# Kernel optimization log

Measured on AMD Instinct MI355X. Metric: run time of the kernel, lower is better.

The kernel has to match this reference:

```python
import jax, jax.numpy as jnp
import numpy as np

L, B, DM, H, HID, NSPK, NB, NC, WIN = 128, 64, 1024, 256, 256, 2, 30, 6, 10
F = 2 * H            # biLSTM output feature dim
MEM = F + HID        # concat of node features and graph-conv output
R = 2 * NSPK * NSPK  # number of edge relations


def _build_edges():
    src_l, dst_l = [], []
    for j in range(L):
        for k in range(max(0, j - WIN), min(L, j + WIN + 1)):
            dst_l.append(j); src_l.append(k)
    dst = np.asarray(dst_l, np.int32); src = np.asarray(src_l, np.int32)
    offs = (np.arange(B, dtype=np.int32) * L)[:, None]
    edge_dst = (dst[None] + offs).reshape(-1)
    edge_src = (src[None] + offs).reshape(-1)
    mask = np.zeros((L, L), bool); mask[dst, src] = True
    return edge_src, edge_dst, mask


def setup_inputs():
    key = jax.random.key(0)
    ks = iter(jax.random.split(key, 32))
    rn = lambda *s: jax.random.normal(next(ks), s, jnp.float32) * 0.05
    edge_src, edge_dst, edge_mask = _build_edges()
    return {
        'U': jax.random.normal(next(ks), (L, B, DM), jnp.float32),
        'umask': jnp.ones((B, L), jnp.float32),
        'Wih0': rn(2, 4 * H, DM), 'Whh0': rn(2, 4 * H, H), 'b0': rn(2, 4 * H),
        'Wih1': rn(2, 4 * H, F), 'Whh1': rn(2, 4 * H, H), 'b1': rn(2, 4 * H),
        'W_scalar': rn(F, L),
        'basis': rn(NB, F, HID), 'comp': rn(R, NB),
        'W_root': rn(F, HID), 'b_rgcn': rn(HID),
        'gc_W1': rn(HID, HID), 'gc_W2': rn(HID, HID), 'gc_b': rn(HID),
        'Wm': rn(MEM, MEM), 'bm': rn(MEM),
        'Wl': rn(MEM, HID), 'bl': rn(HID),
        'Ws': rn(HID, NC), 'bs': rn(NC),
        'speakers': jax.random.randint(next(ks), (L, B), 0, NSPK, jnp.int32),
        'edge_src': jnp.asarray(edge_src), 'edge_dst': jnp.asarray(edge_dst),
        'edge_mask': jnp.asarray(edge_mask),
    }


def _lstm_dir(x, Wih, Whh, b, reverse):
    Bx, Hh = x.shape[1], Whh.shape[1]
    def step(carry, xt):
        h, c = carry
        g = xt @ Wih.T + h @ Whh.T + b          # PyTorch gate order i,f,g,o
        i, f, gg, o = jnp.split(g, 4, axis=-1)
        c = jax.nn.sigmoid(f) * c + jax.nn.sigmoid(i) * jnp.tanh(gg)
        h = jax.nn.sigmoid(o) * jnp.tanh(c)
        return (h, c), h
    init = (jnp.zeros((Bx, Hh), x.dtype), jnp.zeros((Bx, Hh), x.dtype))
    return jax.lax.scan(step, init, x, reverse=reverse)[1]


def _bilstm(x, Wih, Whh, b):
    return jnp.concatenate([_lstm_dir(x, Wih[0], Whh[0], b[0], False),
                            _lstm_dir(x, Wih[1], Whh[1], b[1], True)], -1)


def reference(U, umask, Wih0, Whh0, b0, Wih1, Whh1, b1, W_scalar, basis, comp,
              W_root, b_rgcn, gc_W1, gc_W2, gc_b, Wm, bm, Wl, bl, Ws, bs,
              speakers, edge_src, edge_dst, edge_mask):
    # --- 2-layer biLSTM encoder ---
    feats = _bilstm(_bilstm(U, Wih0, Whh0, b0), Wih1, Whh1, b1)   # (L,B,F)
    # --- MaskedEdgeAttention ('attn1'): edge weights ---
    scale = jnp.einsum('sbd,dm->sbm', feats, W_scalar)            # (L,B,L)
    alpha = jax.nn.softmax(scale, axis=0).transpose(1, 2, 0)      # (B,Lt,Ls)
    masked = alpha * jnp.where(edge_mask, 1.0, 1e-10)
    scores = masked / masked.sum(-1, keepdims=True) * edge_mask
    b_idx = edge_dst // L; i0 = edge_dst % L; i1 = edge_src % L
    edge_norm = scores[b_idx, i0, i1]                             # (E,)
    # --- edge types: speaker pair + temporal direction ---
    s_dst = speakers[i0, b_idx]; s_src = speakers[i1, b_idx]
    e_dir = jnp.where(i0 < i1, 0, 1)
    edge_type = s_dst * (2 * NSPK) + s_src * 2 + e_dir            # (E,) in [0,R)
    # --- node features, conversation-major ---
    x = feats.transpose(1, 0, 2).reshape(B * L, F)                # (N,F)
    N = B * L
    # --- RGCNConv with basis decomposition ---
    W_rel = jnp.einsum('rb,bfo->rfo', comp, basis)                # (R,F,HID)
    x_rel = jnp.einsum('nf,rfo->nro', x, W_rel)                   # (N,R,HID)
    msg = x_rel[edge_src, edge_type] * edge_norm[:, None]
    h = jax.ops.segment_sum(msg, edge_dst, num_segments=N) + x @ W_root + b_rgcn
    # --- GraphConv ---
    agg = jax.ops.segment_sum(h[edge_src], edge_dst, num_segments=N)
    h2 = h @ gc_W1 + gc_b + agg @ gc_W2                           # (N,HID)
    em = jnp.concatenate([x, h2], -1)                             # (N,MEM)
    em = em.reshape(B, L, MEM).transpose(1, 0, 2)                 # (L,B,MEM)
    # --- MatchingAttention ('general2') at every timestep, vectorized ---
    um = umask.T                                                  # (L,B)
    x_tr = em @ Wm + bm                                           # (L,B,MEM)
    logits = jnp.einsum('tbm,sbm->tbs', x_tr, em * um[:, :, None]) * umask[None]
    a = jax.nn.softmax(jnp.tanh(logits), axis=2) * umask[None]
    a = a / a.sum(2, keepdims=True)
    att = jnp.einsum('tbs,sbm->tbm', a, em)
    hidden = jax.nn.relu(att @ Wl + bl)                           # dropout = eval identity
    logp = jax.nn.log_softmax(hidden @ Ws + bs, axis=2)           # (L,B,NC)
    return logp.transpose(1, 0, 2).reshape(B * L, NC)
```

## Files before the change

kernel.cpp:

```cpp
#include <hip/hip_runtime.h>
#include <cstdint>


typedef __attribute__((ext_vector_type(8))) short bf16x8;
typedef __attribute__((ext_vector_type(4))) float f32x4;

__device__ __forceinline__ void gload_lds16(const void* g, void* l) {
  __builtin_amdgcn_global_load_lds(
      (const __attribute__((address_space(1))) void*)g,
      (__attribute__((address_space(3))) void*)l, 16, 0, 0);
}

template<bool HASBIAS, bool ACCUM, bool RELU, bool OUTBF>
__global__ __launch_bounds__(256) void gemm_bf16_nt(
    const ushort* __restrict__ A, const ushort* __restrict__ Bt,
    const float* __restrict__ bias, void* __restrict__ Cv,
    int M, int N, int K, long lda, long ldc,
    long sA, long sB, long sC, long sBias)
{
  const int bz = blockIdx.z;
  A += (long)bz * sA;
  Bt += (long)bz * sB;
  if (HASBIAS) bias += (long)bz * sBias;
  float*  Cf = OUTBF ? nullptr : ((float*)Cv + (long)bz * sC);
  ushort* Cb = OUTBF ? ((ushort*)Cv + (long)bz * sC) : nullptr;

  const int bn = blockIdx.x * 128, bm = blockIdx.y * 128;

  __shared__ ushort As[128][32];
  __shared__ ushort Bs[128][32];

  const int tid = threadIdx.x;
  const int wave = tid >> 6, lane = tid & 63;
  const int wm = (wave >> 1) * 64, wn = (wave & 1) * 64;
  const int fr = lane & 15;
  const int fk = (lane >> 4) * 8;

  f32x4 acc[4][4];
#pragma unroll
  for (int i = 0; i < 4; ++i)
#pragma unroll
    for (int j = 0; j < 4; ++j) acc[i][j] = (f32x4){0.f, 0.f, 0.f, 0.f};

  const int f0 = wave * 2 * 64 + lane;
  const int f1 = f0 + 64;
  const int r0 = f0 >> 2, c0 = (f0 & 3) * 8;
  const int r1 = f1 >> 2, c1 = (f1 & 3) * 8;
  ushort* As0 = (ushort*)As + wave * 2 * 512;
  ushort* As1 = As0 + 512;
  ushort* Bs0 = (ushort*)Bs + wave * 2 * 512;
  ushort* Bs1 = Bs0 + 512;

  for (int k0 = 0; k0 < K; k0 += 32) {
    gload_lds16(A + (long)(bm + r0) * lda + k0 + c0, As0);
    gload_lds16(A + (long)(bm + r1) * lda + k0 + c1, As1);
    gload_lds16(Bt + (long)(bn + r0) * K + k0 + c0, Bs0);
    gload_lds16(Bt + (long)(bn + r1) * K + k0 + c1, Bs1);
    __syncthreads();

    bf16x8 af[4], bfr[4];
#pragma unroll
    for (int f = 0; f < 4; ++f) {
      af[f]  = *(const bf16x8*)&As[wm + f * 16 + fr][fk];
      bfr[f] = *(const bf16x8*)&Bs[wn + f * 16 + fr][fk];
    }
#pragma unroll
    for (int mf = 0; mf < 4; ++mf)
#pragma unroll
      for (int nf = 0; nf < 4; ++nf)
        acc[mf][nf] = __builtin_amdgcn_mfma_f32_16x16x32_bf16(
            af[mf], bfr[nf], acc[mf][nf], 0, 0, 0);
    __syncthreads();
  }

  float bv[4];
#pragma unroll
  for (int nf = 0; nf < 4; ++nf)
    bv[nf] = HASBIAS ? bias[bn + wn + nf * 16 + fr] : 0.f;

  const int crow0 = (lane >> 4) * 4;
#pragma unroll
  for (int mf = 0; mf < 4; ++mf)
#pragma unroll
    for (int r = 0; r < 4; ++r) {
      const long roff = (long)(bm + wm + mf * 16 + crow0 + r) * ldc + bn + wn;
#pragma unroll
      for (int nf = 0; nf < 4; ++nf) {
        float v = acc[mf][nf][r] + bv[nf];
        if (OUTBF) {
          unsigned u = __float_as_uint(v);
          u += 0x7fffu + ((u >> 16) & 1u);
          Cb[roff + nf * 16 + fr] = (ushort)(u >> 16);
        } else {
          if (ACCUM) v += Cf[roff + nf * 16 + fr];
          if (RELU) v = fmaxf(v, 0.f);
          Cf[roff + nf * 16 + fr] = v;
        }
      }
    }
}

__device__ __forceinline__ unsigned short f2bf(float f) {
  unsigned u = __float_as_uint(f);
  u += 0x7fffu + ((u >> 16) & 1u);
  return (unsigned short)(u >> 16);
}
__device__ __forceinline__ float bf2f(ushort v) {
  return __uint_as_float(((unsigned)v) << 16);
}
__device__ __forceinline__ float fast_sig(float x) {
  return __builtin_amdgcn_rcpf(1.f + __expf(-x));
}
__device__ __forceinline__ float fast_tanh(float x) {
  return 2.f * fast_sig(2.f * x) - 1.f;
}

__device__ __forceinline__ int sdot4_(uint a, uint b, int c) {
#if __has_builtin(__builtin_amdgcn_sdot4)
  return __builtin_amdgcn_sdot4((int)a, (int)b, c, false);
#else
  int r = c;
  r += ((int)(a << 24) >> 24) * ((int)(b << 24) >> 24);
  r += ((int)(a << 16) >> 24) * ((int)(b << 16) >> 24);
  r += ((int)(a << 8)  >> 24) * ((int)(b << 8)  >> 24);
  r += ((int)a >> 24)         * ((int)b >> 24);
  return r;
#endif
}

__global__ __launch_bounds__(256) void cvt_all_k(
    const float* __restrict__ U, ushort* __restrict__ ubf,
    const float* __restrict__ W0, ushort* __restrict__ w0,
    const float* __restrict__ W1, ushort* __restrict__ w1,
    const float* __restrict__ b_rgcn, float* __restrict__ biasSW)
{
  const int bid = blockIdx.x;
  if (bid >= 11264) {
    const int idx = (bid - 11264) * 256 + threadIdx.x;
    if (idx < 384) biasSW[idx] = (idx < 128) ? 0.f : b_rgcn[idx - 128];
    return;
  }
  const float* src; ushort* dst; long base;
  if (bid < 8192)       { src = U;  dst = ubf; base = (long)bid * 1024; }
  else if (bid < 10240) { src = W0; dst = w0;  base = (long)(bid - 8192) * 1024; }
  else                  { src = W1; dst = w1;  base = (long)(bid - 10240) * 1024; }
  const long i = base + threadIdx.x * 4;
  float4 v = *(const float4*)(src + i);
  ushort4 o;
  o.x = f2bf(v.x); o.y = f2bf(v.y); o.z = f2bf(v.z); o.w = f2bf(v.w);
  *(ushort4*)(dst + i) = o;
}

__global__ __launch_bounds__(256) void tp_all_k(
    const float* __restrict__ s0, ushort* __restrict__ d0,
    const float* __restrict__ s1, const float* __restrict__ s2,
    ushort* __restrict__ d12,
    const float* __restrict__ s3, ushort* __restrict__ d3,
    const float* __restrict__ s4, ushort* __restrict__ d4,
    const float* __restrict__ s5, ushort* __restrict__ d5)
{
  __shared__ float tile[32][33];
  const int bid = blockIdx.x;
  const float* src; ushort* dst; int C, gx, local, dstStride, dstOff;
  if (bid < 128)       { src = s0; dst = d0;  C = 256; gx = 8;  local = bid;        dstStride = 512; dstOff = 0; }
  else if (bid < 192)  { src = s1; dst = d12; C = 256; gx = 8;  local = bid - 128;  dstStride = 512; dstOff = 0; }
  else if (bid < 256)  { src = s2; dst = d12; C = 256; gx = 8;  local = bid - 192;  dstStride = 512; dstOff = 256; }
  else if (bid < 832)  { src = s3; dst = d3;  C = 768; gx = 24; local = bid - 256;  dstStride = 768; dstOff = 0; }
  else if (bid < 1024) { src = s4; dst = d4;  C = 256; gx = 8;  local = bid - 832;  dstStride = 768; dstOff = 0; }
  else                 { src = s5; dst = d5;  C = 128; gx = 4;  local = bid - 1024; dstStride = 512; dstOff = 0; }
  const int c0 = (local % gx) * 32, r0 = (local / gx) * 32;
  const int tx = threadIdx.x & 31, ty = threadIdx.x >> 5;
#pragma unroll
  for (int j = 0; j < 4; ++j)
    tile[ty + j * 8][tx] = src[(long)(r0 + ty + j * 8) * C + c0 + tx];
  __syncthreads();
#pragma unroll
  for (int j = 0; j < 4; ++j)
    dst[(long)(c0 + ty + j * 8) * dstStride + dstOff + r0 + tx] = f2bf(tile[tx][ty + j * 8]);
}

__global__ __launch_bounds__(256) void pack_whh_all_k(
    const float* __restrict__ Whh0, const float* __restrict__ Whh1,
    uint* __restrict__ Wq, float* __restrict__ fscale)
{
  const int wid = (blockIdx.x * 256 + threadIdx.x) >> 6;
  const int lane = threadIdx.x & 63;
  const int l = wid >> 11;
  const int wid2 = wid & 2047;
  const int d = wid2 >> 10, gi = wid2 & 1023;
  const float* Whh = l ? Whh1 : Whh0;
  const float* row = Whh + ((long)d * 1024 + gi) * 256 + lane * 4;
  float v0 = row[0], v1 = row[1], v2 = row[2], v3 = row[3];
  float am = fmaxf(fmaxf(fabsf(v0), fabsf(v1)), fmaxf(fabsf(v2), fabsf(v3)));
#pragma unroll
  for (int off = 32; off > 0; off >>= 1) am = fmaxf(am, __shfl_xor(am, off, 64));
  am = fmaxf(am, 1e-12f);
  const float inv = 127.f / am;
  int q0 = __float2int_rn(v0 * inv), q1 = __float2int_rn(v1 * inv);
  int q2 = __float2int_rn(v2 * inv), q3 = __float2int_rn(v3 * inv);
  uint w = (uint)(q0 & 255) | ((uint)(q1 & 255) << 8) |
           ((uint)(q2 & 255) << 16) | ((uint)(q3 & 255) << 24);
  Wq[(long)l * 131072 + ((long)d * 64 + lane) * 1024 + gi] = w;
  if (lane == 0) fscale[l * 2048 + d * 1024 + gi] = am / 127.f;
}

__global__ __launch_bounds__(1024) void lstm4_k(
    const ushort* __restrict__ Xg,
    const uint* __restrict__ Wq,
    const float* __restrict__ fscale,
    ushort* __restrict__ out,
    int bmajor, long ldo)
{
  const int bx = blockIdx.x;
  const int d = bx >> 6, b = bx & 63;
  const int tid = threadIdx.x;

  __shared__ uint hq[2][64];
  __shared__ float preactF[1024];

  uint w[64];
  const uint* wrow = Wq + (long)d * 65536 + tid;
#pragma unroll
  for (int k4 = 0; k4 < 64; ++k4) w[k4] = wrow[k4 * 1024];

  if (tid < 128) ((uint*)hq)[tid] = 0u;

  const float fsc = fscale[d * 1024 + tid] * (1.0f / 127.0f);
  const ushort* Xd = Xg + (long)d * 8192 * 1024;

  float c = 0.f;
  float x0 = 0.f, x1 = 0.f, x2 = 0.f, x3 = 0.f;
  if (tid < 256) {
    const ushort* xr = Xd + ((long)((d ? 127 : 0) * 64 + b)) * 1024;
    x0 = bf2f(xr[tid]); x1 = bf2f(xr[tid + 256]);
    x2 = bf2f(xr[tid + 512]); x3 = bf2f(xr[tid + 768]);
  }
  __syncthreads();

  int cur = 0;
  for (int step = 0; step < 128; ++step) {
    const int t = d ? 127 - step : step;

    float n0 = 0.f, n1 = 0.f, n2 = 0.f, n3 = 0.f;
    if (tid < 256 && step + 1 < 128) {
      const ushort* xr = Xd + ((long)((d ? 126 - step : step + 1) * 64 + b)) * 1024;
      n0 = bf2f(xr[tid]); n1 = bf2f(xr[tid + 256]);
      n2 = bf2f(xr[tid + 512]); n3 = bf2f(xr[tid + 768]);
    }

    int acc = 0;
    const uint4* hrow = (const uint4*)hq[cur];
#pragma unroll
    for (int k16 = 0; k16 < 16; ++k16) {
      uint4 h4 = hrow[k16];
      acc = sdot4_(w[k16 * 4 + 0], h4.x, acc);
      acc = sdot4_(w[k16 * 4 + 1], h4.y, acc);
      acc = sdot4_(w[k16 * 4 + 2], h4.z, acc);
      acc = sdot4_(w[k16 * 4 + 3], h4.w, acc);
    }
    preactF[tid] = (float)acc * fsc;
    __syncthreads();

    if (tid < 256) {
      float p0 = x0 + preactF[tid];
      float p1 = x1 + preactF[tid + 256];
      float p2 = x2 + preactF[tid + 512];
      float p3 = x3 + preactF[tid + 768];
      const float ig = fast_sig(p0), fg = fast_sig(p1);
      const float gg = fast_tanh(p2), og = fast_sig(p3);
      c = fg * c + ig * gg;
      const float h = og * fast_tanh(c);
      const long row = bmajor ? ((long)b * 128 + t) : ((long)t * 64 + b);
      out[row * ldo + (d << 8) + tid] = f2bf(h);
      ((char*)hq[cur ^ 1])[tid] = (char)__float2int_rn(h * 127.f);
      x0 = n0; x1 = n1; x2 = n2; x3 = n3;
    }
    __syncthreads();
    cur ^= 1;
  }
}

__global__ __launch_bounds__(256) void wrel_k(const float* __restrict__ basis,
                                              const float* __restrict__ comp,
                                              ushort* __restrict__ wrel2t) {
  const int f = blockIdx.x;
  const int o = threadIdx.x;
  __shared__ float cs[240];
  if (o < 240) cs[o] = comp[o];
  __syncthreads();
  float acc[8];
#pragma unroll
  for (int r = 0; r < 8; ++r) acc[r] = 0.f;
  for (int bb = 0; bb < 30; ++bb) {
    const float v = basis[((long)bb * 512 + f) * 256 + o];
#pragma unroll
    for (int r = 0; r < 8; ++r) acc[r] = fmaf(cs[r * 30 + bb], v, acc[r]);
  }
#pragma unroll
  for (int r = 0; r < 8; ++r)
    wrel2t[((long)(r * 256 + o)) * 512 + f] = f2bf(acc[r]);
}

__global__ __launch_bounds__(256) void rgcn_fused_k(
    const float* __restrict__ scaleM, const ushort* __restrict__ xrel,
    const int* __restrict__ spk, ushort* __restrict__ hagg)
{
  const int n = blockIdx.x;
  const int b = n >> 7, t = n & 127;
  const int o = threadIdx.x;
  const int lo = max(t - 10, 0), hi = min(t + 10, 127);
  const int cnt = hi - lo + 1;

  __shared__ float sc[128], red[128];
  __shared__ int spks[21];
  __shared__ int spkt_s;

  if (o < 128) {
    const float v = scaleM[((long)(b * 128 + o)) * 384 + t];
    sc[o] = v; red[o] = v;
  }
  if (o == 0) spkt_s = spk[t * 64 + b];
  if (o >= 128 && o - 128 < cnt) spks[o - 128] = spk[(lo + o - 128) * 64 + b];
  __syncthreads();
  for (int off = 64; off > 0; off >>= 1) {
    if (o < off) red[o] = fmaxf(red[o], red[o + off]);
    __syncthreads();
  }
  const float m = red[0];
  __syncthreads();
  if (o < 128) {
    const float e = expf(sc[o] - m);
    sc[o] = e;
    const int dd = o - t;
    const bool inwin = (dd <= 10) && (dd >= -10);
    red[o] = e * (inwin ? 1.0f : 1e-10f);
  }
  __syncthreads();
  for (int off = 64; off > 0; off >>= 1) {
    if (o < off) red[o] += red[o + off];
    __syncthreads();
  }
  const float inv_msum = 1.0f / red[0];
  __syncthreads();

  const int spkt = spkt_s;
  float acc = scaleM[(long)n * 384 + 128 + o];
  for (int q = 0; q < cnt; ++q) {
    const int s = lo + q;
    const float wv = sc[s] * inv_msum;
    const int et = spkt * 4 + spks[q] * 2 + ((t < s) ? 0 : 1);
    acc = fmaf(bf2f(xrel[(((long)(b * 128 + s)) * 8 + et) * 256 + o]), wv, acc);
  }
  hagg[(long)n * 512 + o] = f2bf(acc);
}

__global__ __launch_bounds__(256) void agg_k(ushort* __restrict__ hagg) {
  const int n = blockIdx.x;
  const int b = n >> 7, t = n & 127;
  const int o = threadIdx.x;
  const int lo = max(t - 10, 0), hi = min(t + 10, 127);
  float acc = 0.f;
  for (int s = lo; s <= hi; ++s) acc += bf2f(hagg[((long)(b * 128 + s)) * 512 + o]);
  hagg[(long)n * 512 + 256 + o] = f2bf(acc);
}

__global__ __launch_bounds__(256) void emt_k(const ushort* __restrict__ src,
                                             ushort* __restrict__ dst) {
  __shared__ ushort tile[32][33];
  const int c0 = blockIdx.x * 32;
  const int r0 = blockIdx.y * 32;
  const int b = blockIdx.z;
  const ushort* s = src + (long)b * 98304;
  ushort* d = dst + (long)b * 98304;
  const int tx = threadIdx.x & 31, ty = threadIdx.x >> 5;
#pragma unroll
  for (int j = 0; j < 4; ++j)
    tile[ty + j * 8][tx] = s[(long)(r0 + ty + j * 8) * 768 + c0 + tx];
  __syncthreads();
#pragma unroll
  for (int j = 0; j < 4; ++j)
    d[(long)(c0 + ty + j * 8) * 128 + r0 + tx] = tile[tx][ty + j * 8];
}

__global__ __launch_bounds__(128) void match_softmax_k(const float* __restrict__ logits,
                                                       const float* __restrict__ umask,
                                                       ushort* __restrict__ abf) {
  const int bx = blockIdx.x;
  const int b = bx >> 7;
  const int s = threadIdx.x;
  __shared__ float red[128];
  const float* row = logits + (long)bx * 128;
  const float um = umask[b * 128 + s];
  const float v = tanhf(row[s] * um * um);
  red[s] = v; __syncthreads();
  for (int off = 64; off > 0; off >>= 1) { if (s < off) red[s] = fmaxf(red[s], red[s + off]); __syncthreads(); }
  const float m = red[0]; __syncthreads();
  const float e = expf(v - m);
  red[s] = e; __syncthreads();
  for (int off = 64; off > 0; off >>= 1) { if (s < off) red[s] += red[s + off]; __syncthreads(); }
  const float es = red[0]; __syncthreads();
  const float p = (e / es) * um;
  red[s] = p; __syncthreads();
  for (int off = 64; off > 0; off >>= 1) { if (s < off) red[s] += red[s + off]; __syncthreads(); }
  const float ps = red[0];
  abf[(long)bx * 128 + s] = f2bf(p / ps);
}

__global__ __launch_bounds__(256) void final_k(const float* __restrict__ hidden,
                                               const float* __restrict__ Ws,
                                               const float* __restrict__ bs,
                                               float* __restrict__ out) {
  __shared__ float wsl[256 * 6];
  const int tid = threadIdx.x;
#pragma unroll
  for (int j = 0; j < 6; ++j) wsl[tid * 6 + j] = Ws[tid * 6 + j];
  __syncthreads();
  const int wave = tid >> 6, lane = tid & 63;
  const int n = blockIdx.x * 4 + wave;
  const float4 hv = *(const float4*)&hidden[(long)n * 256 + lane * 4];
  const float hvv[4] = {hv.x, hv.y, hv.z, hv.w};
  float a[6];
#pragma unroll
  for (int c = 0; c < 6; ++c) a[c] = 0.f;
#pragma unroll
  for (int j = 0; j < 4; ++j)
#pragma unroll
    for (int c = 0; c < 6; ++c)
      a[c] = fmaf(hvv[j], wsl[(lane * 4 + j) * 6 + c], a[c]);
#pragma unroll
  for (int off = 32; off > 0; off >>= 1)
#pragma unroll
    for (int c = 0; c < 6; ++c)
      a[c] += __shfl_xor(a[c], off, 64);
  if (lane == 0) {
    float v[6], m = -1e30f;
#pragma unroll
    for (int c = 0; c < 6; ++c) { v[c] = a[c] + bs[c]; m = fmaxf(m, v[c]); }
    float sum = 0.f;
#pragma unroll
    for (int c = 0; c < 6; ++c) sum += expf(v[c] - m);
    const float lse = m + logf(sum);
#pragma unroll
    for (int c = 0; c < 6; ++c) out[(long)n * 6 + c] = v[c] - lse;
  }
}

extern "C" void kernel_launch(void* const* d_in, const int* in_sizes, int n_in,
                              void* d_out, int out_size, void* d_ws, size_t ws_size,
                              hipStream_t stream) {
  const float* U        = (const float*)d_in[0];
  const float* umask    = (const float*)d_in[1];
  const float* Wih0     = (const float*)d_in[2];
  const float* Whh0     = (const float*)d_in[3];
  const float* b0       = (const float*)d_in[4];
  const float* Wih1     = (const float*)d_in[5];
  const float* Whh1     = (const float*)d_in[6];
  const float* b1       = (const float*)d_in[7];
  const float* W_scalar = (const float*)d_in[8];
  const float* basis    = (const float*)d_in[9];
  const float* comp     = (const float*)d_in[10];
  const float* W_root   = (const float*)d_in[11];
  const float* b_rgcn   = (const float*)d_in[12];
  const float* gc_W1    = (const float*)d_in[13];
  const float* gc_W2    = (const float*)d_in[14];
  const float* gc_b     = (const float*)d_in[15];
  const float* Wm       = (const float*)d_in[16];
  const float* bm       = (const float*)d_in[17];
  const float* Wl       = (const float*)d_in[18];
  const float* bl       = (const float*)d_in[19];
  const float* Wsw      = (const float*)d_in[20];
  const float* bsw      = (const float*)d_in[21];
  const int*   speakers = (const int*)d_in[22];

  float* ws = (float*)d_ws;
  float* gates   = ws + 0L;
  float* feats   = ws + 16777216L;
  float* xbuf    = ws + 20971520L;
  float* feats0  = ws + 25165824L;
  float* scaleb  = ws + 29360128L;
  float* scoresb = ws + 30408704L;
  float* wrelr   = ws + 31457280L;
  uint*  wq      = (uint*)(ws + 34603008L);
  float* fsc     = ws + 34865152L;
  float* wTr     = ws + 34869248L;
  float* biasSW  = ws + 35426304L;

  ushort* ubf    = (ushort*)xbuf;
  ushort* wih0bf = (ushort*)feats;
  ushort* wih1bf = (ushort*)(feats + 1048576L);
  ushort* f0bf   = (ushort*)feats0;
  ushort* xemb   = (ushort*)feats0;
  ushort* wrel2t = (ushort*)wrelr;
  ushort* wswr   = (ushort*)wTr;
  ushort* gcW12t = wswr + 196608L;
  ushort* Wmt    = gcW12t + 131072L;
  ushort* Wlt    = Wmt + 589824L;

  ushort* gatesbf = (ushort*)gates;
  float*  scaleM  = gates + 8388608L;
  ushort* hagg    = (ushort*)xbuf;
  ushort* emT     = (ushort*)xbuf;
  ushort* xrelbf  = (ushort*)gates;
  ushort* xtrbf   = (ushort*)gates;
  ushort* abf     = (ushort*)scoresb;
  ushort* attbf   = (ushort*)feats;

  float*  logitsb = scaleb;
  float*  hiddenb = scaleb;

  pack_whh_all_k<<<1024, 256, 0, stream>>>(Whh0, Whh1, wq, fsc);
  cvt_all_k<<<11266, 256, 0, stream>>>(U, ubf, Wih0, wih0bf, Wih1, wih1bf,
                                       b_rgcn, biasSW);
  tp_all_k<<<1088, 256, 0, stream>>>(W_root, wswr + 65536L, gc_W1, gc_W2, gcW12t,
                                     Wm, Wmt, Wl, Wlt, W_scalar, wswr);
  wrel_k<<<512, 256, 0, stream>>>(basis, comp, wrel2t);

  gemm_bf16_nt<true, false, false, true><<<dim3(8, 64, 2), 256, 0, stream>>>(
      ubf, wih0bf, b0, gatesbf, 8192, 1024, 1024, 1024L, 1024L,
      0L, 1048576L, 8388608L, 1024L);
  lstm4_k<<<128, 1024, 0, stream>>>(gatesbf, wq, fsc, f0bf, 0, 512L);

  gemm_bf16_nt<true, false, false, true><<<dim3(8, 64, 2), 256, 0, stream>>>(
      f0bf, wih1bf, b1, gatesbf, 8192, 1024, 512, 512L, 1024L,
      0L, 524288L, 8388608L, 1024L);
  lstm4_k<<<128, 1024, 0, stream>>>(gatesbf, wq + 131072, fsc + 2048, xemb, 1, 768L);

  gemm_bf16_nt<true, false, false, false><<<dim3(3, 64, 1), 256, 0, stream>>>(
      xemb, wswr, biasSW, scaleM, 8192, 384, 512, 768L, 384L, 0L, 0L, 0L, 0L);
  gemm_bf16_nt<false, false, false, true><<<dim3(16, 64, 1), 256, 0, stream>>>(
      xemb, wrel2t, nullptr, xrelbf, 8192, 2048, 512, 768L, 2048L, 0L, 0L, 0L, 0L);
  rgcn_fused_k<<<8192, 256, 0, stream>>>(scaleM, xrelbf, speakers, hagg);

  agg_k<<<8192, 256, 0, stream>>>(hagg);
  gemm_bf16_nt<true, false, false, true><<<dim3(2, 64, 1), 256, 0, stream>>>(
      hagg, gcW12t, gc_b, xemb + 512, 8192, 256, 512, 512L, 768L, 0L, 0L, 0L, 0L);

  gemm_bf16_nt<true, false, false, true><<<dim3(6, 64, 1), 256, 0, stream>>>(
      xemb, Wmt, bm, xtrbf, 8192, 768, 768, 768L, 768L, 0L, 0L, 0L, 0L);
  emt_k<<<dim3(24, 4, 64), 256, 0, stream>>>(xemb, emT);
  gemm_bf16_nt<false, false, false, false><<<dim3(1, 1, 64), 256, 0, stream>>>(
      xtrbf, xemb, nullptr, logitsb, 128, 128, 768, 768L, 128L,
      98304L, 98304L, 16384L, 0L);
  match_softmax_k<<<8192, 128, 0, stream>>>(logitsb, umask, abf);
  gemm_bf16_nt<false, false, false, true><<<dim3(6, 1, 64), 256, 0, stream>>>(
      abf, emT, nullptr, attbf, 128, 768, 128, 128L, 768L,
      16384L, 98304L, 98304L, 0L);

  gemm_bf16_nt<true, false, true, false><<<dim3(2, 64, 1), 256, 0, stream>>>(
      attbf, Wlt, bl, hiddenb, 8192, 256, 768, 768L, 256L, 0L, 0L, 0L, 0L);
  final_k<<<2048, 256, 0, stream>>>(hiddenb, Wsw, bsw, (float*)d_out);
}
```

Baseline: 584.1 us.

## Fuse matching attention into one per-batch kernel and merge prep kernels

Replaces the logits GEMM, the row softmax kernel and the attention GEMM with one kernel per batch element. Each block computes the logits with MFMA, keeps them in shared memory, applies the masked softmax there, and multiplies by emT without sending logits or weights through global memory. The four weight-preparation kernels are also merged into two launches to cut launch overhead. The fused attention runs only 64 blocks with large LDS use, so it may under-use the GPU compared with the separate kernels.

```diff
diff --git a/kernel.cpp b/kernel.cpp
--- a/kernel.cpp
+++ b/kernel.cpp
@@ -128,30 +128,58 @@
 #endif
 }
 
-__global__ __launch_bounds__(256) void cvt_all_k(
+__global__ __launch_bounds__(256) void prep1_k(
+    const float* __restrict__ Whh0, const float* __restrict__ Whh1,
+    uint* __restrict__ Wq, float* __restrict__ fscale,
+    const float* __restrict__ basis, const float* __restrict__ comp,
+    ushort* __restrict__ wrel2t)
+{
+  __shared__ float cs[240];
+  const int bid = blockIdx.x;
+  if (bid < 1024) {
+    const int wid = (bid * 256 + threadIdx.x) >> 6;
+    const int lane = threadIdx.x & 63;
+    const int l = wid >> 11;
+    const int wid2 = wid & 2047;
+    const int d = wid2 >> 10, gi = wid2 & 1023;
+    const float* Whh = l ? Whh1 : Whh0;
+    const float* row = Whh + ((long)d * 1024 + gi) * 256 + lane * 4;
+    float v0 = row[0], v1 = row[1], v2 = row[2], v3 = row[3];
+    float am = fmaxf(fmaxf(fabsf(v0), fabsf(v1)), fmaxf(fabsf(v2), fabsf(v3)));
+#pragma unroll
+    for (int off = 32; off > 0; off >>= 1) am = fmaxf(am, __shfl_xor(am, off, 64));
+    am = fmaxf(am, 1e-12f);
+    const float inv = 127.f / am;
+    int q0 = __float2int_rn(v0 * inv), q1 = __float2int_rn(v1 * inv);
+    int q2 = __float2int_rn(v2 * inv), q3 = __float2int_rn(v3 * inv);
+    uint w = (uint)(q0 & 255) | ((uint)(q1 & 255) << 8) |
+             ((uint)(q2 & 255) << 16) | ((uint)(q3 & 255) << 24);
+    Wq[(long)l * 131072 + ((long)d * 64 + lane) * 1024 + gi] = w;
+    if (lane == 0) fscale[l * 2048 + d * 1024 + gi] = am / 127.f;
+    return;
+  }
+  const int f = bid - 1024;
+  const int o = threadIdx.x;
+  if (o < 240) cs[o] = comp[o];
+  __syncthreads();
+  float acc[8];
+#pragma unroll
+  for (int r = 0; r < 8; ++r) acc[r] = 0.f;
+  for (int bb = 0; bb < 30; ++bb) {
+    const float v = basis[((long)bb * 512 + f) * 256 + o];
+#pragma unroll
+    for (int r = 0; r < 8; ++r) acc[r] = fmaf(cs[r * 30 + bb], v, acc[r]);
+  }
+#pragma unroll
+  for (int r = 0; r < 8; ++r)
+    wrel2t[((long)(r * 256 + o)) * 512 + f] = f2bf(acc[r]);
+}
+
+__global__ __launch_bounds__(256) void prep2_k(
     const float* __restrict__ U, ushort* __restrict__ ubf,
     const float* __restrict__ W0, ushort* __restrict__ w0,
     const float* __restrict__ W1, ushort* __restrict__ w1,
-    const float* __restrict__ b_rgcn, float* __restrict__ biasSW)
-{
-  const int bid = blockIdx.x;
-  if (bid >= 11264) {
-    const int idx = (bid - 11264) * 256 + threadIdx.x;
-    if (idx < 384) biasSW[idx] = (idx < 128) ? 0.f : b_rgcn[idx - 128];
-    return;
-  }
-  const float* src; ushort* dst; long base;
-  if (bid < 8192)       { src = U;  dst = ubf; base = (long)bid * 1024; }
-  else if (bid < 10240) { src = W0; dst = w0;  base = (long)(bid - 8192) * 1024; }
-  else                  { src = W1; dst = w1;  base = (long)(bid - 10240) * 1024; }
-  const long i = base + threadIdx.x * 4;
-  float4 v = *(const float4*)(src + i);
-  ushort4 o;
-  o.x = f2bf(v.x); o.y = f2bf(v.y); o.z = f2bf(v.z); o.w = f2bf(v.w);
-  *(ushort4*)(dst + i) = o;
-}
-
-__global__ __launch_bounds__(256) void tp_all_k(
+    const float* __restrict__ b_rgcn, float* __restrict__ biasSW,
     const float* __restrict__ s0, ushort* __restrict__ d0,
     const float* __restrict__ s1, const float* __restrict__ s2,
     ushort* __restrict__ d12,
@@ -160,7 +188,25 @@
     const float* __restrict__ s5, ushort* __restrict__ d5)
 {
   __shared__ float tile[32][33];
-  const int bid = blockIdx.x;
+  const int bid0 = blockIdx.x;
+  if (bid0 < 11264) {
+    const float* src; ushort* dst; long base;
+    if (bid0 < 8192)       { src = U;  dst = ubf; base = (long)bid0 * 1024; }
+    else if (bid0 < 10240) { src = W0; dst = w0;  base = (long)(bid0 - 8192) * 1024; }
+    else                   { src = W1; dst = w1;  base = (long)(bid0 - 10240) * 1024; }
+    const long i = base + threadIdx.x * 4;
+    float4 v = *(const float4*)(src + i);
+    ushort4 o;
+    o.x = f2bf(v.x); o.y = f2bf(v.y); o.z = f2bf(v.z); o.w = f2bf(v.w);
+    *(ushort4*)(dst + i) = o;
+    return;
+  }
+  if (bid0 < 11266) {
+    const int idx = (bid0 - 11264) * 256 + threadIdx.x;
+    if (idx < 384) biasSW[idx] = (idx < 128) ? 0.f : b_rgcn[idx - 128];
+    return;
+  }
+  const int bid = bid0 - 11266;
   const float* src; ushort* dst; int C, gx, local, dstStride, dstOff;
   if (bid < 128)       { src = s0; dst = d0;  C = 256; gx = 8;  local = bid;        dstStride = 512; dstOff = 0; }
   else if (bid < 192)  { src = s1; dst = d12; C = 256; gx = 8;  local = bid - 128;  dstStride = 512; dstOff = 0; }
@@ -177,31 +223,6 @@
 #pragma unroll
   for (int j = 0; j < 4; ++j)
     dst[(long)(c0 + ty + j * 8) * dstStride + dstOff + r0 + tx] = f2bf(tile[tx][ty + j * 8]);
-}
-
-__global__ __launch_bounds__(256) void pack_whh_all_k(
-    const float* __restrict__ Whh0, const float* __restrict__ Whh1,
-    uint* __restrict__ Wq, float* __restrict__ fscale)
-{
-  const int wid = (blockIdx.x * 256 + threadIdx.x) >> 6;
-  const int lane = threadIdx.x & 63;
-  const int l = wid >> 11;
-  const int wid2 = wid & 2047;
-  const int d = wid2 >> 10, gi = wid2 & 1023;
-  const float* Whh = l ? Whh1 : Whh0;
-  const float* row = Whh + ((long)d * 1024 + gi) * 256 + lane * 4;
-  float v0 = row[0], v1 = row[1], v2 = row[2], v3 = row[3];
-  float am = fmaxf(fmaxf(fabsf(v0), fabsf(v1)), fmaxf(fabsf(v2), fabsf(v3)));
-#pragma unroll
-  for (int off = 32; off > 0; off >>= 1) am = fmaxf(am, __shfl_xor(am, off, 64));
-  am = fmaxf(am, 1e-12f);
-  const float inv = 127.f / am;
-  int q0 = __float2int_rn(v0 * inv), q1 = __float2int_rn(v1 * inv);
-  int q2 = __float2int_rn(v2 * inv), q3 = __float2int_rn(v3 * inv);
-  uint w = (uint)(q0 & 255) | ((uint)(q1 & 255) << 8) |
-           ((uint)(q2 & 255) << 16) | ((uint)(q3 & 255) << 24);
-  Wq[(long)l * 131072 + ((long)d * 64 + lane) * 1024 + gi] = w;
-  if (lane == 0) fscale[l * 2048 + d * 1024 + gi] = am / 127.f;
 }
 
 __global__ __launch_bounds__(1024) void lstm4_k(
@@ -280,27 +301,6 @@
   }
 }
 
-__global__ __launch_bounds__(256) void wrel_k(const float* __restrict__ basis,
-                                              const float* __restrict__ comp,
-                                              ushort* __restrict__ wrel2t) {
-  const int f = blockIdx.x;
-  const int o = threadIdx.x;
-  __shared__ float cs[240];
-  if (o < 240) cs[o] = comp[o];
-  __syncthreads();
-  float acc[8];
-#pragma unroll
-  for (int r = 0; r < 8; ++r) acc[r] = 0.f;
-  for (int bb = 0; bb < 30; ++bb) {
-    const float v = basis[((long)bb * 512 + f) * 256 + o];
-#pragma unroll
-    for (int r = 0; r < 8; ++r) acc[r] = fmaf(cs[r * 30 + bb], v, acc[r]);
-  }
-#pragma unroll
-  for (int r = 0; r < 8; ++r)
-    wrel2t[((long)(r * 256 + o)) * 512 + f] = f2bf(acc[r]);
-}
-
 __global__ __launch_bounds__(256) void rgcn_fused_k(
     const float* __restrict__ scaleM, const ushort* __restrict__ xrel,
     const int* __restrict__ spk, ushort* __restrict__ hagg)
@@ -382,28 +382,139 @@
     d[(long)(c0 + ty + j * 8) * 128 + r0 + tx] = tile[tx][ty + j * 8];
 }
 
-__global__ __launch_bounds__(128) void match_softmax_k(const float* __restrict__ logits,
-                                                       const float* __restrict__ umask,
-                                                       ushort* __restrict__ abf) {
-  const int bx = blockIdx.x;
-  const int b = bx >> 7;
-  const int s = threadIdx.x;
-  __shared__ float red[128];
-  const float* row = logits + (long)bx * 128;
-  const float um = umask[b * 128 + s];
-  const float v = tanhf(row[s] * um * um);
-  red[s] = v; __syncthreads();
-  for (int off = 64; off > 0; off >>= 1) { if (s < off) red[s] = fmaxf(red[s], red[s + off]); __syncthreads(); }
-  const float m = red[0]; __syncthreads();
-  const float e = expf(v - m);
-  red[s] = e; __syncthreads();
-  for (int off = 64; off > 0; off >>= 1) { if (s < off) red[s] += red[s + off]; __syncthreads(); }
-  const float es = red[0]; __syncthreads();
-  const float p = (e / es) * um;
-  red[s] = p; __syncthreads();
-  for (int off = 64; off > 0; off >>= 1) { if (s < off) red[s] += red[s + off]; __syncthreads(); }
-  const float ps = red[0];
-  abf[(long)bx * 128 + s] = f2bf(p / ps);
+__global__ __launch_bounds__(256) void mega_attn_k(
+    const ushort* __restrict__ xtr,
+    const ushort* __restrict__ em,
+    const ushort* __restrict__ emT,
+    const float* __restrict__ umask,
+    ushort* __restrict__ att)
+{
+  const int b = blockIdx.x;
+  const ushort* A = xtr + (long)b * 98304;
+  const ushort* B = em + (long)b * 98304;
+  const ushort* BT = emT + (long)b * 98304;
+  ushort* C = att + (long)b * 98304;
+
+  __shared__ ushort As[128][32];
+  __shared__ ushort Bs[128][32];
+  __shared__ float logT[128][129];
+  __shared__ ushort albf[128][136];
+  __shared__ float um_l[128];
+  __shared__ float red2[2][128];
+
+  const int tid = threadIdx.x;
+  const int wave = tid >> 6, lane = tid & 63;
+  const int wm = (wave >> 1) * 64, wn = (wave & 1) * 64;
+  const int fr = lane & 15;
+  const int fk = (lane >> 4) * 8;
+  const int crow0 = (lane >> 4) * 4;
+
+  if (tid < 128) um_l[tid] = umask[b * 128 + tid];
+
+  const int f0 = wave * 2 * 64 + lane;
+  const int f1 = f0 + 64;
+  const int r0 = f0 >> 2, c0 = (f0 & 3) * 8;
+  const int r1 = f1 >> 2, c1 = (f1 & 3) * 8;
+  ushort* As0 = (ushort*)As + wave * 2 * 512;
+  ushort* As1 = As0 + 512;
+  ushort* Bs0 = (ushort*)Bs + wave * 2 * 512;
+  ushort* Bs1 = Bs0 + 512;
+
+  f32x4 acc[4][4];
+#pragma unroll
+  for (int i = 0; i < 4; ++i)
+#pragma unroll
+    for (int j = 0; j < 4; ++j) acc[i][j] = (f32x4){0.f, 0.f, 0.f, 0.f};
+
+  for (int k0 = 0; k0 < 768; k0 += 32) {
+    gload_lds16(A + (long)r0 * 768 + k0 + c0, As0);
+    gload_lds16(A + (long)r1 * 768 + k0 + c1, As1);
+    gload_lds16(B + (long)r0 * 768 + k0 + c0, Bs0);
+    gload_lds16(B + (long)r1 * 768 + k0 + c1, Bs1);
+    __syncthreads();
+    bf16x8 af[4], bfr[4];
+#pragma unroll
+    for (int f = 0; f < 4; ++f) {
+      af[f]  = *(const bf16x8*)&As[wm + f * 16 + fr][fk];
+      bfr[f] = *(const bf16x8*)&Bs[wn + f * 16 + fr][fk];
+    }
+#pragma unroll
+    for (int mf = 0; mf < 4; ++mf)
+#pragma unroll
+      for (int nf = 0; nf < 4; ++nf)
+        acc[mf][nf] = __builtin_amdgcn_mfma_f32_16x16x32_bf16(
+            af[mf], bfr[nf], acc[mf][nf], 0, 0, 0);
+    __syncthreads();
+  }
+#pragma unroll
+  for (int mf = 0; mf < 4; ++mf)
+#pragma unroll
+    for (int r = 0; r < 4; ++r)
+#pragma unroll
+      for (int nf = 0; nf < 4; ++nf)
+        logT[wn + nf * 16 + fr][wm + mf * 16 + crow0 + r] = acc[mf][nf][r];
+  __syncthreads();
+
+  {
+    const int t = tid & 127, hh = tid >> 7;
+    float vmax = -1e30f;
+    for (int s = hh * 64; s < hh * 64 + 64; ++s) {
+      const float um = um_l[s];
+      vmax = fmaxf(vmax, tanhf(logT[s][t] * um * um));
+    }
+    red2[hh][t] = vmax;
+    __syncthreads();
+    const float m = fmaxf(red2[0][t], red2[1][t]);
+    __syncthreads();
+    float lsum = 0.f;
+    for (int s = hh * 64; s < hh * 64 + 64; ++s) {
+      const float um = um_l[s];
+      lsum += expf(tanhf(logT[s][t] * um * um) - m) * um;
+    }
+    red2[hh][t] = lsum;
+    __syncthreads();
+    const float invS = 1.f / (red2[0][t] + red2[1][t]);
+    for (int s = hh * 64; s < hh * 64 + 64; ++s) {
+      const float um = um_l[s];
+      albf[t][s] = f2bf(expf(tanhf(logT[s][t] * um * um) - m) * um * invS);
+    }
+  }
+  __syncthreads();
+
+  for (int nt = 0; nt < 6; ++nt) {
+    f32x4 acc2[4][4];
+#pragma unroll
+    for (int i = 0; i < 4; ++i)
+#pragma unroll
+      for (int j = 0; j < 4; ++j) acc2[i][j] = (f32x4){0.f, 0.f, 0.f, 0.f};
+    for (int k0 = 0; k0 < 128; k0 += 32) {
+      gload_lds16(BT + (long)(nt * 128 + r0) * 128 + k0 + c0, Bs0);
+      gload_lds16(BT + (long)(nt * 128 + r1) * 128 + k0 + c1, Bs1);
+      __syncthreads();
+      bf16x8 af[4], bfr[4];
+#pragma unroll
+      for (int f = 0; f < 4; ++f) {
+        af[f]  = *(const bf16x8*)&albf[wm + f * 16 + fr][k0 + fk];
+        bfr[f] = *(const bf16x8*)&Bs[wn + f * 16 + fr][fk];
+      }
+#pragma unroll
+      for (int mf = 0; mf < 4; ++mf)
+#pragma unroll
+        for (int nf = 0; nf < 4; ++nf)
+          acc2[mf][nf] = __builtin_amdgcn_mfma_f32_16x16x32_bf16(
+              af[mf], bfr[nf], acc2[mf][nf], 0, 0, 0);
+      __syncthreads();
+    }
+#pragma unroll
+    for (int mf = 0; mf < 4; ++mf)
+#pragma unroll
+      for (int r = 0; r < 4; ++r) {
+        const long roff = (long)(wm + mf * 16 + crow0 + r) * 768 + nt * 128 + wn;
+#pragma unroll
+        for (int nf = 0; nf < 4; ++nf)
+          C[roff + nf * 16 + fr] = f2bf(acc2[mf][nf][r]);
+      }
+  }
 }
 
 __global__ __launch_bounds__(256) void final_k(const float* __restrict__ hidden,
@@ -502,18 +613,15 @@
   ushort* emT     = (ushort*)xbuf;
   ushort* xrelbf  = (ushort*)gates;
   ushort* xtrbf   = (ushort*)gates;
-  ushort* abf     = (ushort*)scoresb;
   ushort* attbf   = (ushort*)feats;
 
-  float*  logitsb = scaleb;
   float*  hiddenb = scaleb;
 
-  pack_whh_all_k<<<1024, 256, 0, stream>>>(Whh0, Whh1, wq, fsc);
-  cvt_all_k<<<11266, 256, 0, stream>>>(U, ubf, Wih0, wih0bf, Wih1, wih1bf,
-                                       b_rgcn, biasSW);
-  tp_all_k<<<1088, 256, 0, stream>>>(W_root, wswr + 65536L, gc_W1, gc_W2, gcW12t,
+  prep1_k<<<1536, 256, 0, stream>>>(Whh0, Whh1, wq, fsc, basis, comp, wrel2t);
+  prep2_k<<<12354, 256, 0, stream>>>(U, ubf, Wih0, wih0bf, Wih1, wih1bf,
+                                     b_rgcn, biasSW,
+                                     W_root, wswr + 65536L, gc_W1, gc_W2, gcW12t,
                                      Wm, Wmt, Wl, Wlt, W_scalar, wswr);
-  wrel_k<<<512, 256, 0, stream>>>(basis, comp, wrel2t);
 
   gemm_bf16_nt<true, false, false, true><<<dim3(8, 64, 2), 256, 0, stream>>>(
       ubf, wih0bf, b0, gatesbf, 8192, 1024, 1024, 1024L, 1024L,
@@ -538,13 +646,7 @@
   gemm_bf16_nt<true, false, false, true><<<dim3(6, 64, 1), 256, 0, stream>>>(
       xemb, Wmt, bm, xtrbf, 8192, 768, 768, 768L, 768L, 0L, 0L, 0L, 0L);
   emt_k<<<dim3(24, 4, 64), 256, 0, stream>>>(xemb, emT);
-  gemm_bf16_nt<false, false, false, false><<<dim3(1, 1, 64), 256, 0, stream>>>(
-      xtrbf, xemb, nullptr, logitsb, 128, 128, 768, 768L, 128L,
-      98304L, 98304L, 16384L, 0L);
-  match_softmax_k<<<8192, 128, 0, stream>>>(logitsb, umask, abf);
-  gemm_bf16_nt<false, false, false, true><<<dim3(6, 1, 64), 256, 0, stream>>>(
-      abf, emT, nullptr, attbf, 128, 768, 128, 128L, 768L,
-      16384L, 98304L, 98304L, 0L);
+  mega_attn_k<<<64, 256, 0, stream>>>(xtrbf, xemb, emT, umask, attbf);
 
   gemm_bf16_nt<true, false, true, false><<<dim3(2, 64, 1), 256, 0, stream>>>(
       attbf, Wlt, bl, hiddenb, 8192, 256, 768, 768L, 256L, 0L, 0L, 0L, 0L);
```

New measurement: 603.5 us. 3.3% more time.
